# Kernel tuning notes

Hardware: AMD Instinct MI355X
Metric: run time of the kernel (lower is better)

The kernel has to match this reference:

```python
import jax, jax.numpy as jnp
import numpy as np

H = 128
B = 512
T = 1024
FUT = 64


def setup_inputs() -> dict:
    key = jax.random.key(0)
    ks = jax.random.split(key, 11)
    k = 1.0 / np.sqrt(H)  # torch LSTMCell/Linear init range
    u = lambda kk, shape: jax.random.uniform(kk, shape, jnp.float32, -k, k)
    return {
        "x": jax.random.normal(ks[0], (B, T), jnp.float32),
        "W_ih1": u(ks[1], (4 * H, 1)),
        "b_ih1": u(ks[2], (4 * H,)),
        "W_hh1": u(ks[3], (4 * H, H)),
        "b_hh1": u(ks[4], (4 * H,)),
        "W_ih2": u(ks[5], (4 * H, H)),
        "b_ih2": u(ks[6], (4 * H,)),
        "W_hh2": u(ks[7], (4 * H, H)),
        "b_hh2": u(ks[8], (4 * H,)),
        "W_out": u(ks[9], (1, H)),
        "b_out": u(ks[10], (1,)),
        "future": FUT,
    }


def _cell(x_t, h, c, W_ih, b_ih, W_hh, b_hh):
    # torch.nn.LSTMCell: gates ordered i, f, g, o
    g = x_t @ W_ih.T + h @ W_hh.T + (b_ih + b_hh)
    i, f, gg, o = jnp.split(g, 4, axis=-1)
    c_new = jax.nn.sigmoid(f) * c + jax.nn.sigmoid(i) * jnp.tanh(gg)
    h_new = jax.nn.sigmoid(o) * jnp.tanh(c_new)
    return h_new, c_new


def reference(x, W_ih1, b_ih1, W_hh1, b_hh1, W_ih2, b_ih2, W_hh2, b_hh2, W_out, b_out, future):
    Bn = x.shape[0]
    Hn = W_hh1.shape[1]
    z = jnp.zeros((Bn, Hn), x.dtype)

    def enc_step(carry, x_t):
        h1, c1, h2, c2 = carry
        h1, c1 = _cell(x_t, h1, c1, W_ih1, b_ih1, W_hh1, b_hh1)
        h2, c2 = _cell(h1, h2, c2, W_ih2, b_ih2, W_hh2, b_hh2)
        return (h1, c1, h2, c2), None

    xs = x.T[:, :, None]  # [T, B, 1]
    (h1, c1, h2, c2), _ = jax.lax.scan(enc_step, (z, z, z, z), xs)
    out0 = h2 @ W_out.T + b_out  # [B, 1]

    def fut_step(carry, _):
        h1, c1, h2, c2, out = carry
        h1, c1 = _cell(out, h1, c1, W_ih1, b_ih1, W_hh1, b_hh1)
        h2, c2 = _cell(h1, h2, c2, W_ih2, b_ih2, W_hh2, b_hh2)
        out = h2 @ W_out.T + b_out
        return (h1, c1, h2, c2, out), out

    _, fouts = jax.lax.scan(fut_step, (h1, c1, h2, c2, out0), None, length=future - 1)
    # torch cats [B,1] tensors on dim=1 -> [B, future]
    return jnp.concatenate([out0, fouts[:, :, 0].T], axis=1)
```

## Files before the change

### kernel.cpp

```cpp
#include <hip/hip_runtime.h>

#define HH 128
#define TT 1024
#define NFUT 64
#define MB 2
#define NBLK 256
#define NITER (TT + NFUT)

typedef _Float16 half8 __attribute__((ext_vector_type(8)));
typedef float floatx4 __attribute__((ext_vector_type(4)));

#define MFMA16(a, b, c) __builtin_amdgcn_mfma_f32_16x16x32_f16((a), (b), (c), 0, 0, 0)
#define SFENCE() __builtin_amdgcn_sched_barrier(0)

__device__ __forceinline__ float sigm(float v) {
  return __builtin_amdgcn_rcpf(1.0f + __builtin_amdgcn_exp2f(v * -1.442695040888963f));
}
__device__ __forceinline__ float tanh_f(float v) {
  float a = __builtin_fabsf(v);
  float e = __builtin_amdgcn_exp2f(a * -2.885390081777927f);
  float r = (1.0f - e) * __builtin_amdgcn_rcpf(1.0f + e);
  return __builtin_copysignf(r, v);
}
__device__ __forceinline__ half8 ldw8(const float* __restrict__ p) {
  half8 r;
#pragma unroll
  for (int i = 0; i < 8; ++i) r[i] = (_Float16)p[i];
  return r;
}

__global__
__attribute__((amdgpu_flat_work_group_size(512, 512), amdgpu_waves_per_eu(2, 2)))
void lstm_kernel(
    const float* __restrict__ x,
    const float* __restrict__ W_ih1, const float* __restrict__ b_ih1,
    const float* __restrict__ W_hh1, const float* __restrict__ b_hh1,
    const float* __restrict__ W_ih2, const float* __restrict__ b_ih2,
    const float* __restrict__ W_hh2, const float* __restrict__ b_hh2,
    const float* __restrict__ W_out, const float* __restrict__ b_out,
    float* __restrict__ out)
{
  __shared__ __align__(16) _Float16 h1b[2][2048];
  __shared__ __align__(16) _Float16 h2b[2][2048];
  __shared__ float xs[TT * MB];
  __shared__ float opart[8 * MB];

  const int tid = (int)threadIdx.x;
  const int lane = tid & 63;
  const int w = tid >> 6;
  const int jl = lane & 15;
  const int rg = lane >> 4;
  const int j = w * 16 + jl;
  const int b0g = (int)blockIdx.x * MB;

  for (int idx = tid; idx < TT * MB; idx += 512) {
    int t = idx & (TT - 1);
    int bb = idx >> 10;
    xs[t * MB + bb] = x[(b0g + bb) * TT + t];
  }
  for (int idx = tid; idx < 2 * 2048; idx += 512) {
    h1b[idx >> 11][idx & 2047] = (_Float16)0.0f;
    h2b[idx >> 11][idx & 2047] = (_Float16)0.0f;
  }

  half8 A00, A01, A02, A03, A10, A11, A12, A13, A20, A21, A22, A23, A30, A31, A32, A33;
  half8 H00, H01, H02, H03, H10, H11, H12, H13, H20, H21, H22, H23, H30, H31, H32, H33;
  half8 I00, I01, I02, I03, I10, I11, I12, I13, I20, I21, I22, I23, I30, I31, I32, I33;
#define LDW(N, Q, P) do { \
    const float* _p = (P) + ((Q) * HH + j) * HH + rg * 8; \
    N##0 = ldw8(_p);      N##1 = ldw8(_p + 32); \
    N##2 = ldw8(_p + 64); N##3 = ldw8(_p + 96); } while (0)
  LDW(A0, 0, W_hh1); LDW(A1, 1, W_hh1); LDW(A2, 2, W_hh1); LDW(A3, 3, W_hh1);
  LDW(H0, 0, W_hh2); LDW(H1, 1, W_hh2); LDW(H2, 2, W_hh2); LDW(H3, 3, W_hh2);
  LDW(I0, 0, W_ih2); LDW(I1, 1, W_ih2); LDW(I2, 2, W_ih2); LDW(I3, 3, W_ih2);

  float bias1[4], bias2[4], wi1[4];
#pragma unroll
  for (int q = 0; q < 4; ++q) {
    bias1[q] = b_ih1[q * HH + j] + b_hh1[q * HH + j];
    bias2[q] = b_ih2[q * HH + j] + b_hh2[q * HH + j];
    wi1[q] = W_ih1[q * HH + j];
  }
  const float wo = W_out[j];
  const float bo = b_out[0];
  float c1a = 0.f, c1b = 0.f, c2a = 0.f, c2b = 0.f;

  __syncthreads();

  const int aoff = lane * 8;
  const int wb = ((j >> 5) << 9) + (((j >> 3) & 3) << 7) + (j & 7);

#define G2K(KF) do { \
    half8 bv = *(const half8*)(&h2b[prv][KF * 512 + aoff]); \
    g0 = MFMA16(bv, H0##KF, g0); g1 = MFMA16(bv, H1##KF, g1); \
    g2 = MFMA16(bv, H2##KF, g2); g3 = MFMA16(bv, H3##KF, g3); \
    half8 aw = *(const half8*)(&h1b[prv][KF * 512 + aoff]); \
    g0 = MFMA16(aw, I0##KF, g0); g1 = MFMA16(aw, I1##KF, g1); \
    g2 = MFMA16(aw, I2##KF, g2); g3 = MFMA16(aw, I3##KF, g3); } while (0)
#define G1K(KF) do { \
    half8 av = *(const half8*)(&h1b[prv][KF * 512 + aoff]); \
    a0 = MFMA16(av, A0##KF, a0); a1 = MFMA16(av, A1##KF, a1); \
    a2 = MFMA16(av, A2##KF, a2); a3 = MFMA16(av, A3##KF, a3); } while (0)

  for (int k = 0; k < NITER; ++k) {
    const int cur = k & 1;
    const int prv = cur ^ 1;

    floatx4 g0 = {0.f,0.f,0.f,0.f}, g1 = {0.f,0.f,0.f,0.f};
    floatx4 g2 = {0.f,0.f,0.f,0.f}, g3 = {0.f,0.f,0.f,0.f};
    __builtin_amdgcn_s_setprio(1);
    G2K(0); G2K(1); G2K(2); G2K(3);
    __builtin_amdgcn_s_setprio(0);
    SFENCE();

    if (k >= 1) {
      float gi0 = g0[0] + bias2[0], gi1 = g0[1] + bias2[0];
      float gf0 = g1[0] + bias2[1], gf1 = g1[1] + bias2[1];
      float gg0 = g2[0] + bias2[2], gg1 = g2[1] + bias2[2];
      float go0 = g3[0] + bias2[3], go1 = g3[1] + bias2[3];
      c2a = sigm(gf0) * c2a + sigm(gi0) * tanh_f(gg0);
      c2b = sigm(gf1) * c2b + sigm(gi1) * tanh_f(gg1);
      float h20 = sigm(go0) * tanh_f(c2a);
      float h21 = sigm(go1) * tanh_f(c2b);
      if (lane < 16) {
        h2b[cur][wb] = (_Float16)h20;
        h2b[cur][wb + 8] = (_Float16)h21;
      }
      if (k >= TT) {
        float p0 = h20 * wo, p1 = h21 * wo;
        p0 += __shfl_xor(p0, 1); p1 += __shfl_xor(p1, 1);
        p0 += __shfl_xor(p0, 2); p1 += __shfl_xor(p1, 2);
        p0 += __shfl_xor(p0, 4); p1 += __shfl_xor(p1, 4);
        p0 += __shfl_xor(p0, 8); p1 += __shfl_xor(p1, 8);
        if (lane == 0) {
          opart[w * MB + 0] = p0;
          opart[w * MB + 1] = p1;
        }
      }
    }
    SFENCE();

    floatx4 a0 = {0.f,0.f,0.f,0.f}, a1 = {0.f,0.f,0.f,0.f};
    floatx4 a2 = {0.f,0.f,0.f,0.f}, a3 = {0.f,0.f,0.f,0.f};
    __builtin_amdgcn_s_setprio(1);
    G1K(0); G1K(1); G1K(2); G1K(3);
    __builtin_amdgcn_s_setprio(0);
    SFENCE();

    float x0, x1;
    if (k < TT) {
      x0 = xs[k * MB + 0];
      x1 = xs[k * MB + 1];
    } else {
      __syncthreads();
      float s0 = bo, s1 = bo;
#pragma unroll
      for (int p = 0; p < 8; ++p) {
        s0 += opart[p * MB + 0];
        s1 += opart[p * MB + 1];
      }
      x0 = s0; x1 = s1;
      if (w == 0 && lane < MB) out[(b0g + lane) * NFUT + (k - TT)] = (lane == 0) ? s0 : s1;
    }

    if (k <= NITER - 2) {
      float gi0 = a0[0] + x0 * wi1[0] + bias1[0], gi1 = a0[1] + x1 * wi1[0] + bias1[0];
      float gf0 = a1[0] + x0 * wi1[1] + bias1[1], gf1 = a1[1] + x1 * wi1[1] + bias1[1];
      float gg0 = a2[0] + x0 * wi1[2] + bias1[2], gg1 = a2[1] + x1 * wi1[2] + bias1[2];
      float go0 = a3[0] + x0 * wi1[3] + bias1[3], go1 = a3[1] + x1 * wi1[3] + bias1[3];
      c1a = sigm(gf0) * c1a + sigm(gi0) * tanh_f(gg0);
      c1b = sigm(gf1) * c1b + sigm(gi1) * tanh_f(gg1);
      float h10 = sigm(go0) * tanh_f(c1a);
      float h11 = sigm(go1) * tanh_f(c1b);
      if (lane < 16) {
        h1b[cur][wb] = (_Float16)h10;
        h1b[cur][wb + 8] = (_Float16)h11;
      }
    }
    __syncthreads();
    SFENCE();
  }
}

extern "C" void kernel_launch(void* const* d_in, const int* in_sizes, int n_in,
                              void* d_out, int out_size, void* d_ws, size_t ws_size,
                              hipStream_t stream) {
  const float* x     = (const float*)d_in[0];
  const float* W_ih1 = (const float*)d_in[1];
  const float* b_ih1 = (const float*)d_in[2];
  const float* W_hh1 = (const float*)d_in[3];
  const float* b_hh1 = (const float*)d_in[4];
  const float* W_ih2 = (const float*)d_in[5];
  const float* b_ih2 = (const float*)d_in[6];
  const float* W_hh2 = (const float*)d_in[7];
  const float* b_hh2 = (const float*)d_in[8];
  const float* W_out = (const float*)d_in[9];
  const float* b_out = (const float*)d_in[10];
  (void)in_sizes; (void)n_in; (void)out_size; (void)d_ws; (void)ws_size;

  lstm_kernel<<<dim3(NBLK), dim3(512), 0, stream>>>(
      x, W_ih1, b_ih1, W_hh1, b_hh1, W_ih2, b_ih2, W_hh2, b_hh2, W_out, b_out,
      (float*)d_out);
}
```

Baseline: 1.489 ms.

## Split gate MFMAs into two halves and compute i/f sigmoids between them

```diff
diff --git a/kernel.cpp b/kernel.cpp
--- a/kernel.cpp
+++ b/kernel.cpp
@@ -90,36 +90,41 @@
   const int aoff = lane * 8;
   const int wb = ((j >> 5) << 9) + (((j >> 3) & 3) << 7) + (j & 7);
 
-#define G2K(KF) do { \
+#define G2H(KF, N0, N1) do { \
     half8 bv = *(const half8*)(&h2b[prv][KF * 512 + aoff]); \
-    g0 = MFMA16(bv, H0##KF, g0); g1 = MFMA16(bv, H1##KF, g1); \
-    g2 = MFMA16(bv, H2##KF, g2); g3 = MFMA16(bv, H3##KF, g3); \
+    p0 = MFMA16(bv, H##N0##KF, p0); p1 = MFMA16(bv, H##N1##KF, p1); \
     half8 aw = *(const half8*)(&h1b[prv][KF * 512 + aoff]); \
-    g0 = MFMA16(aw, I0##KF, g0); g1 = MFMA16(aw, I1##KF, g1); \
-    g2 = MFMA16(aw, I2##KF, g2); g3 = MFMA16(aw, I3##KF, g3); } while (0)
-#define G1K(KF) do { \
+    p0 = MFMA16(aw, I##N0##KF, p0); p1 = MFMA16(aw, I##N1##KF, p1); } while (0)
+#define G1H(KF, N0, N1) do { \
     half8 av = *(const half8*)(&h1b[prv][KF * 512 + aoff]); \
-    a0 = MFMA16(av, A0##KF, a0); a1 = MFMA16(av, A1##KF, a1); \
-    a2 = MFMA16(av, A2##KF, a2); a3 = MFMA16(av, A3##KF, a3); } while (0)
+    p0 = MFMA16(av, A##N0##KF, p0); p1 = MFMA16(av, A##N1##KF, p1); } while (0)
 
   for (int k = 0; k < NITER; ++k) {
     const int cur = k & 1;
     const int prv = cur ^ 1;
 
-    floatx4 g0 = {0.f,0.f,0.f,0.f}, g1 = {0.f,0.f,0.f,0.f};
-    floatx4 g2 = {0.f,0.f,0.f,0.f}, g3 = {0.f,0.f,0.f,0.f};
-    __builtin_amdgcn_s_setprio(1);
-    G2K(0); G2K(1); G2K(2); G2K(3);
-    __builtin_amdgcn_s_setprio(0);
-    SFENCE();
-
+    floatx4 p0, p1;
+    float si0, si1, sf0, sf1;
+
+    p0 = (floatx4){0.f,0.f,0.f,0.f}; p1 = (floatx4){0.f,0.f,0.f,0.f};
+    __builtin_amdgcn_s_setprio(1);
+    G2H(0, 0, 1); G2H(1, 0, 1); G2H(2, 0, 1); G2H(3, 0, 1);
+    __builtin_amdgcn_s_setprio(0);
+    SFENCE();
+    si0 = sigm(p0[0] + bias2[0]); si1 = sigm(p0[1] + bias2[0]);
+    sf0 = sigm(p1[0] + bias2[1]); sf1 = sigm(p1[1] + bias2[1]);
+    SFENCE();
+
+    p0 = (floatx4){0.f,0.f,0.f,0.f}; p1 = (floatx4){0.f,0.f,0.f,0.f};
+    __builtin_amdgcn_s_setprio(1);
+    G2H(0, 2, 3); G2H(1, 2, 3); G2H(2, 2, 3); G2H(3, 2, 3);
+    __builtin_amdgcn_s_setprio(0);
+    SFENCE();
     if (k >= 1) {
-      float gi0 = g0[0] + bias2[0], gi1 = g0[1] + bias2[0];
-      float gf0 = g1[0] + bias2[1], gf1 = g1[1] + bias2[1];
-      float gg0 = g2[0] + bias2[2], gg1 = g2[1] + bias2[2];
-      float go0 = g3[0] + bias2[3], go1 = g3[1] + bias2[3];
-      c2a = sigm(gf0) * c2a + sigm(gi0) * tanh_f(gg0);
-      c2b = sigm(gf1) * c2b + sigm(gi1) * tanh_f(gg1);
+      float gg0 = p0[0] + bias2[2], gg1 = p0[1] + bias2[2];
+      float go0 = p1[0] + bias2[3], go1 = p1[1] + bias2[3];
+      c2a = sf0 * c2a + si0 * tanh_f(gg0);
+      c2b = sf1 * c2b + si1 * tanh_f(gg1);
       float h20 = sigm(go0) * tanh_f(c2a);
       float h21 = sigm(go1) * tanh_f(c2b);
       if (lane < 16) {
@@ -127,24 +132,17 @@
         h2b[cur][wb + 8] = (_Float16)h21;
       }
       if (k >= TT) {
-        float p0 = h20 * wo, p1 = h21 * wo;
-        p0 += __shfl_xor(p0, 1); p1 += __shfl_xor(p1, 1);
-        p0 += __shfl_xor(p0, 2); p1 += __shfl_xor(p1, 2);
-        p0 += __shfl_xor(p0, 4); p1 += __shfl_xor(p1, 4);
-        p0 += __shfl_xor(p0, 8); p1 += __shfl_xor(p1, 8);
+        float q0 = h20 * wo, q1 = h21 * wo;
+        q0 += __shfl_xor(q0, 1); q1 += __shfl_xor(q1, 1);
+        q0 += __shfl_xor(q0, 2); q1 += __shfl_xor(q1, 2);
+        q0 += __shfl_xor(q0, 4); q1 += __shfl_xor(q1, 4);
+        q0 += __shfl_xor(q0, 8); q1 += __shfl_xor(q1, 8);
         if (lane == 0) {
-          opart[w * MB + 0] = p0;
-          opart[w * MB + 1] = p1;
+          opart[w * MB + 0] = q0;
+          opart[w * MB + 1] = q1;
         }
       }
     }
-    SFENCE();
-
-    floatx4 a0 = {0.f,0.f,0.f,0.f}, a1 = {0.f,0.f,0.f,0.f};
-    floatx4 a2 = {0.f,0.f,0.f,0.f}, a3 = {0.f,0.f,0.f,0.f};
-    __builtin_amdgcn_s_setprio(1);
-    G1K(0); G1K(1); G1K(2); G1K(3);
-    __builtin_amdgcn_s_setprio(0);
     SFENCE();
 
     float x0, x1;
@@ -162,14 +160,27 @@
       x0 = s0; x1 = s1;
       if (w == 0 && lane < MB) out[(b0g + lane) * NFUT + (k - TT)] = (lane == 0) ? s0 : s1;
     }
-
+    SFENCE();
+
+    p0 = (floatx4){0.f,0.f,0.f,0.f}; p1 = (floatx4){0.f,0.f,0.f,0.f};
+    __builtin_amdgcn_s_setprio(1);
+    G1H(0, 0, 1); G1H(1, 0, 1); G1H(2, 0, 1); G1H(3, 0, 1);
+    __builtin_amdgcn_s_setprio(0);
+    SFENCE();
+    si0 = sigm(p0[0] + x0 * wi1[0] + bias1[0]); si1 = sigm(p0[1] + x1 * wi1[0] + bias1[0]);
+    sf0 = sigm(p1[0] + x0 * wi1[1] + bias1[1]); sf1 = sigm(p1[1] + x1 * wi1[1] + bias1[1]);
+    SFENCE();
+
+    p0 = (floatx4){0.f,0.f,0.f,0.f}; p1 = (floatx4){0.f,0.f,0.f,0.f};
+    __builtin_amdgcn_s_setprio(1);
+    G1H(0, 2, 3); G1H(1, 2, 3); G1H(2, 2, 3); G1H(3, 2, 3);
+    __builtin_amdgcn_s_setprio(0);
+    SFENCE();
     if (k <= NITER - 2) {
-      float gi0 = a0[0] + x0 * wi1[0] + bias1[0], gi1 = a0[1] + x1 * wi1[0] + bias1[0];
-      float gf0 = a1[0] + x0 * wi1[1] + bias1[1], gf1 = a1[1] + x1 * wi1[1] + bias1[1];
-      float gg0 = a2[0] + x0 * wi1[2] + bias1[2], gg1 = a2[1] + x1 * wi1[2] + bias1[2];
-      float go0 = a3[0] + x0 * wi1[3] + bias1[3], go1 = a3[1] + x1 * wi1[3] + bias1[3];
-      c1a = sigm(gf0) * c1a + sigm(gi0) * tanh_f(gg0);
-      c1b = sigm(gf1) * c1b + sigm(gi1) * tanh_f(gg1);
+      float gg0 = p0[0] + x0 * wi1[2] + bias1[2], gg1 = p0[1] + x1 * wi1[2] + bias1[2];
+      float go0 = p1[0] + x0 * wi1[3] + bias1[3], go1 = p1[1] + x1 * wi1[3] + bias1[3];
+      c1a = sf0 * c1a + si0 * tanh_f(gg0);
+      c1b = sf1 * c1b + si1 * tanh_f(gg1);
       float h10 = sigm(go0) * tanh_f(c1a);
       float h11 = sigm(go1) * tanh_f(c1b);
       if (lane < 16) {
```

Result: slower. 1.551 ms (+4.2%).

## Split LSTM gate columns across two wave groups in 1024-thread blocks

Applied to the files above, without the earlier changes.

```diff
diff --git a/kernel.cpp b/kernel.cpp
--- a/kernel.cpp
+++ b/kernel.cpp
@@ -30,7 +30,7 @@
 }
 
 __global__
-__attribute__((amdgpu_flat_work_group_size(512, 512), amdgpu_waves_per_eu(2, 2)))
+__attribute__((amdgpu_flat_work_group_size(1024, 1024), amdgpu_waves_per_eu(4, 4)))
 void lstm_kernel(
     const float* __restrict__ x,
     const float* __restrict__ W_ih1, const float* __restrict__ b_ih1,
@@ -43,44 +43,47 @@
   __shared__ __align__(16) _Float16 h1b[2][2048];
   __shared__ __align__(16) _Float16 h2b[2][2048];
   __shared__ float xs[TT * MB];
+  __shared__ float sif[2][2][2][128];
   __shared__ float opart[8 * MB];
 
   const int tid = (int)threadIdx.x;
   const int lane = tid & 63;
   const int w = tid >> 6;
+  const int gp = w >> 3;
+  const int nw = w & 7;
   const int jl = lane & 15;
   const int rg = lane >> 4;
-  const int j = w * 16 + jl;
+  const int j = nw * 16 + jl;
+  const int q0 = gp * 2, q1 = gp * 2 + 1;
   const int b0g = (int)blockIdx.x * MB;
 
-  for (int idx = tid; idx < TT * MB; idx += 512) {
+  for (int idx = tid; idx < TT * MB; idx += 1024) {
     int t = idx & (TT - 1);
     int bb = idx >> 10;
     xs[t * MB + bb] = x[(b0g + bb) * TT + t];
   }
-  for (int idx = tid; idx < 2 * 2048; idx += 512) {
+  for (int idx = tid; idx < 2 * 2048; idx += 1024) {
     h1b[idx >> 11][idx & 2047] = (_Float16)0.0f;
     h2b[idx >> 11][idx & 2047] = (_Float16)0.0f;
   }
 
-  half8 A00, A01, A02, A03, A10, A11, A12, A13, A20, A21, A22, A23, A30, A31, A32, A33;
-  half8 H00, H01, H02, H03, H10, H11, H12, H13, H20, H21, H22, H23, H30, H31, H32, H33;
-  half8 I00, I01, I02, I03, I10, I11, I12, I13, I20, I21, I22, I23, I30, I31, I32, I33;
+  half8 Aa0, Aa1, Aa2, Aa3, Ab0, Ab1, Ab2, Ab3;
+  half8 Ha0, Ha1, Ha2, Ha3, Hb0, Hb1, Hb2, Hb3;
+  half8 Ia0, Ia1, Ia2, Ia3, Ib0, Ib1, Ib2, Ib3;
 #define LDW(N, Q, P) do { \
     const float* _p = (P) + ((Q) * HH + j) * HH + rg * 8; \
     N##0 = ldw8(_p);      N##1 = ldw8(_p + 32); \
     N##2 = ldw8(_p + 64); N##3 = ldw8(_p + 96); } while (0)
-  LDW(A0, 0, W_hh1); LDW(A1, 1, W_hh1); LDW(A2, 2, W_hh1); LDW(A3, 3, W_hh1);
-  LDW(H0, 0, W_hh2); LDW(H1, 1, W_hh2); LDW(H2, 2, W_hh2); LDW(H3, 3, W_hh2);
-  LDW(I0, 0, W_ih2); LDW(I1, 1, W_ih2); LDW(I2, 2, W_ih2); LDW(I3, 3, W_ih2);
-
-  float bias1[4], bias2[4], wi1[4];
-#pragma unroll
-  for (int q = 0; q < 4; ++q) {
-    bias1[q] = b_ih1[q * HH + j] + b_hh1[q * HH + j];
-    bias2[q] = b_ih2[q * HH + j] + b_hh2[q * HH + j];
-    wi1[q] = W_ih1[q * HH + j];
-  }
+  LDW(Aa, q0, W_hh1); LDW(Ab, q1, W_hh1);
+  LDW(Ha, q0, W_hh2); LDW(Hb, q1, W_hh2);
+  LDW(Ia, q0, W_ih2); LDW(Ib, q1, W_ih2);
+
+  const float b1a = b_ih1[q0 * HH + j] + b_hh1[q0 * HH + j];
+  const float b1b = b_ih1[q1 * HH + j] + b_hh1[q1 * HH + j];
+  const float b2a = b_ih2[q0 * HH + j] + b_hh2[q0 * HH + j];
+  const float b2b = b_ih2[q1 * HH + j] + b_hh2[q1 * HH + j];
+  const float w1a = W_ih1[q0 * HH + j];
+  const float w1b = W_ih1[q1 * HH + j];
   const float wo = W_out[j];
   const float bo = b_out[0];
   float c1a = 0.f, c1b = 0.f, c2a = 0.f, c2b = 0.f;
@@ -90,67 +93,90 @@
   const int aoff = lane * 8;
   const int wb = ((j >> 5) << 9) + (((j >> 3) & 3) << 7) + (j & 7);
 
-#define G2K(KF) do { \
+#define C2K(KF) do { \
     half8 bv = *(const half8*)(&h2b[prv][KF * 512 + aoff]); \
-    g0 = MFMA16(bv, H0##KF, g0); g1 = MFMA16(bv, H1##KF, g1); \
-    g2 = MFMA16(bv, H2##KF, g2); g3 = MFMA16(bv, H3##KF, g3); \
+    p0 = MFMA16(bv, Ha##KF, p0); p1 = MFMA16(bv, Hb##KF, p1); \
     half8 aw = *(const half8*)(&h1b[prv][KF * 512 + aoff]); \
-    g0 = MFMA16(aw, I0##KF, g0); g1 = MFMA16(aw, I1##KF, g1); \
-    g2 = MFMA16(aw, I2##KF, g2); g3 = MFMA16(aw, I3##KF, g3); } while (0)
-#define G1K(KF) do { \
+    p0 = MFMA16(aw, Ia##KF, p0); p1 = MFMA16(aw, Ib##KF, p1); } while (0)
+#define C1K(KF) do { \
     half8 av = *(const half8*)(&h1b[prv][KF * 512 + aoff]); \
-    a0 = MFMA16(av, A0##KF, a0); a1 = MFMA16(av, A1##KF, a1); \
-    a2 = MFMA16(av, A2##KF, a2); a3 = MFMA16(av, A3##KF, a3); } while (0)
+    p0 = MFMA16(av, Aa##KF, p0); p1 = MFMA16(av, Ab##KF, p1); } while (0)
 
   for (int k = 0; k < NITER; ++k) {
     const int cur = k & 1;
     const int prv = cur ^ 1;
-
-    floatx4 g0 = {0.f,0.f,0.f,0.f}, g1 = {0.f,0.f,0.f,0.f};
-    floatx4 g2 = {0.f,0.f,0.f,0.f}, g3 = {0.f,0.f,0.f,0.f};
+    const bool fut = (k >= TT);
+    const bool doC1 = (k <= NITER - 2);
+
+    floatx4 p0 = {0.f,0.f,0.f,0.f}, p1 = {0.f,0.f,0.f,0.f};
     __builtin_amdgcn_s_setprio(1);
-    G2K(0); G2K(1); G2K(2); G2K(3);
+    C2K(0); C2K(1); C2K(2); C2K(3);
     __builtin_amdgcn_s_setprio(0);
     SFENCE();
-
-    if (k >= 1) {
-      float gi0 = g0[0] + bias2[0], gi1 = g0[1] + bias2[0];
-      float gf0 = g1[0] + bias2[1], gf1 = g1[1] + bias2[1];
-      float gg0 = g2[0] + bias2[2], gg1 = g2[1] + bias2[2];
-      float go0 = g3[0] + bias2[3], go1 = g3[1] + bias2[3];
-      c2a = sigm(gf0) * c2a + sigm(gi0) * tanh_f(gg0);
-      c2b = sigm(gf1) * c2b + sigm(gi1) * tanh_f(gg1);
-      float h20 = sigm(go0) * tanh_f(c2a);
-      float h21 = sigm(go1) * tanh_f(c2b);
+    float e20 = p0[0], e21 = p0[1], f20 = p1[0], f21 = p1[1];
+    SFENCE();
+    p0 = (floatx4){0.f,0.f,0.f,0.f}; p1 = (floatx4){0.f,0.f,0.f,0.f};
+    __builtin_amdgcn_s_setprio(1);
+    C1K(0); C1K(1); C1K(2); C1K(3);
+    __builtin_amdgcn_s_setprio(0);
+    SFENCE();
+    float e10 = p0[0], e11 = p0[1], f10 = p1[0], f11 = p1[1];
+
+    float x0 = 0.f, x1 = 0.f;
+    if (!fut) { x0 = xs[k * MB + 0]; x1 = xs[k * MB + 1]; }
+
+    if (gp == 0 && lane < 16) {
+      sif[1][0][0][j] = sigm(e20 + b2a);
+      sif[1][0][1][j] = sigm(e21 + b2a);
+      sif[1][1][0][j] = sigm(f20 + b2b);
+      sif[1][1][1][j] = sigm(f21 + b2b);
+      if (!fut) {
+        sif[0][0][0][j] = sigm(e10 + x0 * w1a + b1a);
+        sif[0][0][1][j] = sigm(e11 + x1 * w1a + b1a);
+        sif[0][1][0][j] = sigm(f10 + x0 * w1b + b1b);
+        sif[0][1][1][j] = sigm(f11 + x1 * w1b + b1b);
+      }
+    }
+    __syncthreads();
+
+    if (gp == 1 && k >= 1) {
+      float si0 = sif[1][0][0][j], si1 = sif[1][0][1][j];
+      float sf0 = sif[1][1][0][j], sf1 = sif[1][1][1][j];
+      c2a = sf0 * c2a + si0 * tanh_f(e20 + b2a);
+      c2b = sf1 * c2b + si1 * tanh_f(e21 + b2a);
+      float h20 = sigm(f20 + b2b) * tanh_f(c2a);
+      float h21 = sigm(f21 + b2b) * tanh_f(c2b);
       if (lane < 16) {
         h2b[cur][wb] = (_Float16)h20;
         h2b[cur][wb + 8] = (_Float16)h21;
       }
-      if (k >= TT) {
-        float p0 = h20 * wo, p1 = h21 * wo;
-        p0 += __shfl_xor(p0, 1); p1 += __shfl_xor(p1, 1);
-        p0 += __shfl_xor(p0, 2); p1 += __shfl_xor(p1, 2);
-        p0 += __shfl_xor(p0, 4); p1 += __shfl_xor(p1, 4);
-        p0 += __shfl_xor(p0, 8); p1 += __shfl_xor(p1, 8);
+      if (fut) {
+        float u0 = h20 * wo, u1 = h21 * wo;
+        u0 += __shfl_xor(u0, 1); u1 += __shfl_xor(u1, 1);
+        u0 += __shfl_xor(u0, 2); u1 += __shfl_xor(u1, 2);
+        u0 += __shfl_xor(u0, 4); u1 += __shfl_xor(u1, 4);
+        u0 += __shfl_xor(u0, 8); u1 += __shfl_xor(u1, 8);
         if (lane == 0) {
-          opart[w * MB + 0] = p0;
-          opart[w * MB + 1] = p1;
+          opart[nw * MB + 0] = u0;
+          opart[nw * MB + 1] = u1;
         }
       }
     }
-    SFENCE();
-
-    floatx4 a0 = {0.f,0.f,0.f,0.f}, a1 = {0.f,0.f,0.f,0.f};
-    floatx4 a2 = {0.f,0.f,0.f,0.f}, a3 = {0.f,0.f,0.f,0.f};
-    __builtin_amdgcn_s_setprio(1);
-    G1K(0); G1K(1); G1K(2); G1K(3);
-    __builtin_amdgcn_s_setprio(0);
-    SFENCE();
-
-    float x0, x1;
-    if (k < TT) {
-      x0 = xs[k * MB + 0];
-      x1 = xs[k * MB + 1];
+
+    if (!fut) {
+      if (gp == 1) {
+        float si0 = sif[0][0][0][j], si1 = sif[0][0][1][j];
+        float sf0 = sif[0][1][0][j], sf1 = sif[0][1][1][j];
+        c1a = sf0 * c1a + si0 * tanh_f(e10 + x0 * w1a + b1a);
+        c1b = sf1 * c1b + si1 * tanh_f(e11 + x1 * w1a + b1a);
+        float h10 = sigm(f10 + x0 * w1b + b1b) * tanh_f(c1a);
+        float h11 = sigm(f11 + x1 * w1b + b1b) * tanh_f(c1b);
+        if (lane < 16) {
+          h1b[cur][wb] = (_Float16)h10;
+          h1b[cur][wb + 8] = (_Float16)h11;
+        }
+      }
+      __syncthreads();
     } else {
       __syncthreads();
       float s0 = bo, s1 = bo;
@@ -161,23 +187,27 @@
       }
       x0 = s0; x1 = s1;
       if (w == 0 && lane < MB) out[(b0g + lane) * NFUT + (k - TT)] = (lane == 0) ? s0 : s1;
+      if (gp == 0 && lane < 16 && doC1) {
+        sif[0][0][0][j] = sigm(e10 + x0 * w1a + b1a);
+        sif[0][0][1][j] = sigm(e11 + x1 * w1a + b1a);
+        sif[0][1][0][j] = sigm(f10 + x0 * w1b + b1b);
+        sif[0][1][1][j] = sigm(f11 + x1 * w1b + b1b);
+      }
+      __syncthreads();
+      if (gp == 1 && doC1) {
+        float si0 = sif[0][0][0][j], si1 = sif[0][0][1][j];
+        float sf0 = sif[0][1][0][j], sf1 = sif[0][1][1][j];
+        c1a = sf0 * c1a + si0 * tanh_f(e10 + x0 * w1a + b1a);
+        c1b = sf1 * c1b + si1 * tanh_f(e11 + x1 * w1a + b1a);
+        float h10 = sigm(f10 + x0 * w1b + b1b) * tanh_f(c1a);
+        float h11 = sigm(f11 + x1 * w1b + b1b) * tanh_f(c1b);
+        if (lane < 16) {
+          h1b[cur][wb] = (_Float16)h10;
+          h1b[cur][wb + 8] = (_Float16)h11;
+        }
+      }
+      __syncthreads();
     }
-
-    if (k <= NITER - 2) {
-      float gi0 = a0[0] + x0 * wi1[0] + bias1[0], gi1 = a0[1] + x1 * wi1[0] + bias1[0];
-      float gf0 = a1[0] + x0 * wi1[1] + bias1[1], gf1 = a1[1] + x1 * wi1[1] + bias1[1];
-      float gg0 = a2[0] + x0 * wi1[2] + bias1[2], gg1 = a2[1] + x1 * wi1[2] + bias1[2];
-      float go0 = a3[0] + x0 * wi1[3] + bias1[3], go1 = a3[1] + x1 * wi1[3] + bias1[3];
-      c1a = sigm(gf0) * c1a + sigm(gi0) * tanh_f(gg0);
-      c1b = sigm(gf1) * c1b + sigm(gi1) * tanh_f(gg1);
-      float h10 = sigm(go0) * tanh_f(c1a);
-      float h11 = sigm(go1) * tanh_f(c1b);
-      if (lane < 16) {
-        h1b[cur][wb] = (_Float16)h10;
-        h1b[cur][wb + 8] = (_Float16)h11;
-      }
-    }
-    __syncthreads();
     SFENCE();
   }
 }
@@ -198,7 +228,7 @@
   const float* b_out = (const float*)d_in[10];
   (void)in_sizes; (void)n_in; (void)out_size; (void)d_ws; (void)ws_size;
 
-  lstm_kernel<<<dim3(NBLK), dim3(512), 0, stream>>>(
+  lstm_kernel<<<dim3(NBLK), dim3(1024), 0, stream>>>(
       x, W_ih1, b_ih1, W_hh1, b_hh1, W_ih2, b_ih2, W_hh2, b_hh2, W_out, b_out,
       (float*)d_out);
 }
```

After: 2.743 ms. 84.3% more time.
